# Performance work log

Hardware: AMD Instinct MI355X
Metric: run time of the kernel (lower is better)

## Reference

```python
import jax, jax.numpy as jnp
import numpy as np

B, S, D, H, E, K, F, FS = 4, 2048, 1024, 16, 8, 2, 4096, 2048
HD = D // H
EPS = 1e-5
T = B * S
CAP = int(1.25 * K * T / E)  # capacity factor 1.25 -> 2560 tokens/expert


def _ln(x, g, b):
    mu = jnp.mean(x, -1, keepdims=True)
    var = jnp.var(x, -1, keepdims=True)
    return (x - mu) * jax.lax.rsqrt(var + EPS) * g + b


def _forward(x, attention_mask, ln1_g, ln1_b, wq, bq, wk, bk, wv, bv, wo, bo,
             ln2_g, ln2_b, w_router, w1, b1, w2, b2, ws1, bs1, ws2, bs2):
    # ---- pre-LN self-attention + residual ----
    xn = _ln(x, ln1_g, ln1_b)
    q = (xn @ wq + bq).reshape(B, S, H, HD)
    k = (xn @ wk + bk).reshape(B, S, H, HD)
    v = (xn @ wv + bv).reshape(B, S, H, HD)
    scores = jnp.einsum('bqhd,bkhd->bhqk', q, k) / np.float32(np.sqrt(HD))
    scores = jnp.where(attention_mask[:, None, None, :], jnp.finfo(scores.dtype).min, scores)
    p = jax.nn.softmax(scores, axis=-1)
    attn = jnp.einsum('bhqk,bkhd->bqhd', p, v).reshape(B, S, D) @ wo + bo
    x = x + attn
    # ---- pre-LN sparse MoE FFN + residual ----
    xn = _ln(x, ln2_g, ln2_b).reshape(T, D)
    logits = xn.astype(jnp.float32) @ w_router              # router in fp32, [T,E]
    probs = jax.nn.softmax(logits, axis=-1)
    topv, topi = jax.lax.top_k(probs, K)                    # [T,K]
    topv = topv / jnp.sum(topv, -1, keepdims=True)          # renormalize top-k gates
    oh = jax.nn.one_hot(topi, E, dtype=jnp.float32)         # [T,K,E]
    flat = oh.transpose(1, 0, 2).reshape(K * T, E)          # slot-major routing priority
    pos_tok = jnp.sum((jnp.cumsum(flat, axis=0) - 1.0) * flat, -1)  # slot position within expert
    keep = pos_tok < CAP                                    # drop tokens over capacity
    posc = jnp.clip(pos_tok, 0, CAP - 1).astype(jnp.int32)
    eidx = topi.T.reshape(K * T)
    w = topv.T.reshape(K * T) * keep
    xt = jnp.tile(xn, (K, 1)) * keep[:, None]               # [K*T, D]
    disp = jnp.zeros((E, CAP, D), xn.dtype).at[eidx, posc].add(xt)   # dispatch [E,C,D]
    h = jax.nn.gelu(jnp.einsum('ecd,edf->ecf', disp, w1) + b1[:, None, :], approximate=False)
    eo = jnp.einsum('ecf,efd->ecd', h, w2) + b2[:, None, :]          # expert out [E,C,D]
    y = jnp.sum(eo[eidx, posc].reshape(K, T, D) * w.reshape(K, T, 1), axis=0)  # combine
    # shared expert (dense, always active)
    y = y + jax.nn.gelu(xn @ ws1 + bs1, approximate=False) @ ws2 + bs2
    return x + y.reshape(B, S, D)


def setup_inputs() -> dict:
    key = jax.random.key(0)
    ks = jax.random.split(key, 16)
    g = lambda k, shape, fan: jax.random.normal(k, shape, jnp.float32) * (fan ** -0.5)
    return {
        'x': jax.random.normal(ks[0], (B, S, D), jnp.float32),
        'attention_mask': jnp.zeros((B, S), bool),
        'ln1_g': jnp.ones((D,), jnp.float32), 'ln1_b': jnp.zeros((D,), jnp.float32),
        'wq': g(ks[1], (D, D), D), 'bq': jnp.zeros((D,), jnp.float32),
        'wk': g(ks[2], (D, D), D), 'bk': jnp.zeros((D,), jnp.float32),
        'wv': g(ks[3], (D, D), D), 'bv': jnp.zeros((D,), jnp.float32),
        'wo': g(ks[4], (D, D), D), 'bo': jnp.zeros((D,), jnp.float32),
        'ln2_g': jnp.ones((D,), jnp.float32), 'ln2_b': jnp.zeros((D,), jnp.float32),
        'w_router': g(ks[5], (D, E), D),
        'w1': g(ks[6], (E, D, F), D), 'b1': jnp.zeros((E, F), jnp.float32),
        'w2': g(ks[7], (E, F, D), F), 'b2': jnp.zeros((E, D), jnp.float32),
        'ws1': g(ks[8], (D, FS), D), 'bs1': jnp.zeros((FS,), jnp.float32),
        'ws2': g(ks[9], (FS, D), FS), 'bs2': jnp.zeros((D,), jnp.float32),
    }


def reference(x, attention_mask, ln1_g, ln1_b, wq, bq, wk, bk, wv, bv, wo, bo,
              ln2_g, ln2_b, w_router, w1, b1, w2, b2, ws1, bs1, ws2, bs2):
    return _forward(x, attention_mask, ln1_g, ln1_b, wq, bq, wk, bk, wv, bv, wo, bo,
                    ln2_g, ln2_b, w_router, w1, b1, w2, b2, ws1, bs1, ws2, bs2)
```

## Files before the change

kernel.cpp:

```cpp
#include <hip/hip_runtime.h>
#include <hip/hip_bf16.h>
#include <stdint.h>

#define D_ 1024
#define S_ 2048
#define B_ 4
#define H_ 16
#define T_ 8192
#define E_ 8
#define CAP_ 2560
#define F_ 4096
#define FS_ 2048

typedef __attribute__((ext_vector_type(8))) short s8v;
typedef __attribute__((ext_vector_type(4))) float f4v;

#define GLL(gp, lp) __builtin_amdgcn_global_load_lds( \
    (const __attribute__((address_space(1))) unsigned int*)(gp), \
    (__attribute__((address_space(3))) unsigned int*)(lp), 16, 0, 0)

__device__ inline short f2bf(float f) {
    union { float f; unsigned u; } v; v.f = f;
    unsigned r = (v.u + 0x7fffu + ((v.u >> 16) & 1u)) >> 16;
    return (short)(r & 0xffffu);
}
__device__ inline float b2f(short h) {
    union { unsigned u; float f; } v; v.u = ((unsigned)(unsigned short)h) << 16; return v.f;
}
__device__ inline float gelu_f(float x) {
    return 0.5f * x * (1.0f + erff(x * 0.7071067811865475f));
}
__device__ inline f4v f4zero() { f4v z; z[0]=0.f; z[1]=0.f; z[2]=0.f; z[3]=0.f; return z; }

__device__ inline unsigned pk2(float a, float b, unsigned* lo) {
    const short ha = f2bf(a), hb = f2bf(b);
    const short la = f2bf(a - b2f(ha)), lb = f2bf(b - b2f(hb));
    *lo = ((unsigned)(unsigned short)lb << 16) | (unsigned)(unsigned short)la;
    return ((unsigned)(unsigned short)hb << 16) | (unsigned)(unsigned short)ha;
}

__global__ __launch_bounds__(256) void transcvt(const float* __restrict__ in,
                                                short* __restrict__ out, int R, int C)
{
    __shared__ float tile[32][33];
    const int tid = threadIdx.x;
    const int tx = tid & 31, ty = tid >> 5;
    const long long ib = (long long)blockIdx.z * R * C;
    const int r0 = blockIdx.y * 32, c0 = blockIdx.x * 32;
#pragma unroll
    for (int i = 0; i < 4; i++)
        tile[ty + i * 8][tx] = in[ib + (long long)(r0 + ty + i * 8) * C + c0 + tx];
    __syncthreads();
#pragma unroll
    for (int i = 0; i < 4; i++)
        out[ib + (long long)(c0 + ty + i * 8) * R + r0 + tx] = f2bf(tile[tx][ty + i * 8]);
}

__global__ __launch_bounds__(256) void transcvt2(const float* __restrict__ in,
    short* __restrict__ oh, short* __restrict__ ol, int R, int C)
{
    __shared__ float tile[32][33];
    const int tid = threadIdx.x;
    const int tx = tid & 31, ty = tid >> 5;
    const int r0 = blockIdx.y * 32, c0 = blockIdx.x * 32;
#pragma unroll
    for (int i = 0; i < 4; i++)
        tile[ty + i * 8][tx] = in[(long long)(r0 + ty + i * 8) * C + c0 + tx];
    __syncthreads();
#pragma unroll
    for (int i = 0; i < 4; i++) {
        const float v = tile[tx][ty + i * 8];
        const short h = f2bf(v);
        const long long o = (long long)(c0 + ty + i * 8) * R + r0 + tx;
        oh[o] = h;
        ol[o] = f2bf(v - b2f(h));
    }
}

__global__ __launch_bounds__(256) void ln1_split(const float* __restrict__ x,
    const float* __restrict__ g, const float* __restrict__ bta,
    short* __restrict__ xh, short* __restrict__ xl)
{
    const int t = blockIdx.x, tid = threadIdx.x;
    const float4 v = ((const float4*)(x + (long long)t * D_))[tid];
    float s1 = v.x + v.y + v.z + v.w;
    float s2 = v.x * v.x + v.y * v.y + v.z * v.z + v.w * v.w;
#pragma unroll
    for (int off = 32; off; off >>= 1) { s1 += __shfl_xor(s1, off, 64); s2 += __shfl_xor(s2, off, 64); }
    __shared__ float r1[4], r2[4];
    if ((tid & 63) == 0) { r1[tid >> 6] = s1; r2[tid >> 6] = s2; }
    __syncthreads();
    s1 = r1[0] + r1[1] + r1[2] + r1[3];
    s2 = r2[0] + r2[1] + r2[2] + r2[3];
    const float mu = s1 * (1.0f / D_);
    const float var = s2 * (1.0f / D_) - mu * mu;
    const float rs = rsqrtf(var + 1e-5f);
    const float4 gv = ((const float4*)g)[tid];
    const float4 bv = ((const float4*)bta)[tid];
    float xn[4];
    xn[0] = (v.x - mu) * rs * gv.x + bv.x;
    xn[1] = (v.y - mu) * rs * gv.y + bv.y;
    xn[2] = (v.z - mu) * rs * gv.z + bv.z;
    xn[3] = (v.w - mu) * rs * gv.w + bv.w;
    short4 hh, ll;
    hh.x = f2bf(xn[0]); ll.x = f2bf(xn[0] - b2f(hh.x));
    hh.y = f2bf(xn[1]); ll.y = f2bf(xn[1] - b2f(hh.y));
    hh.z = f2bf(xn[2]); ll.z = f2bf(xn[2] - b2f(hh.z));
    hh.w = f2bf(xn[3]); ll.w = f2bf(xn[3] - b2f(hh.w));
    ((short4*)(xh + (long long)t * D_))[tid] = hh;
    ((short4*)(xl + (long long)t * D_))[tid] = ll;
}

__global__ __launch_bounds__(256) void ln2_router_kernel(const float* __restrict__ x,
    const float* __restrict__ g, const float* __restrict__ bta, const float* __restrict__ wr,
    short* __restrict__ xo, int* __restrict__ topi, float* __restrict__ gates)
{
    const int t = blockIdx.x, tid = threadIdx.x;
    const float4 v = ((const float4*)(x + (long long)t * D_))[tid];
    float s1 = v.x + v.y + v.z + v.w;
    float s2 = v.x * v.x + v.y * v.y + v.z * v.z + v.w * v.w;
#pragma unroll
    for (int off = 32; off; off >>= 1) { s1 += __shfl_xor(s1, off, 64); s2 += __shfl_xor(s2, off, 64); }
    __shared__ float r1[4], r2[4];
    if ((tid & 63) == 0) { r1[tid >> 6] = s1; r2[tid >> 6] = s2; }
    __syncthreads();
    s1 = r1[0] + r1[1] + r1[2] + r1[3];
    s2 = r2[0] + r2[1] + r2[2] + r2[3];
    const float mu = s1 * (1.0f / D_);
    const float var = s2 * (1.0f / D_) - mu * mu;
    const float rs = rsqrtf(var + 1e-5f);
    const float4 gv = ((const float4*)g)[tid];
    const float4 bv = ((const float4*)bta)[tid];
    float xn[4];
    xn[0] = (v.x - mu) * rs * gv.x + bv.x;
    xn[1] = (v.y - mu) * rs * gv.y + bv.y;
    xn[2] = (v.z - mu) * rs * gv.z + bv.z;
    xn[3] = (v.w - mu) * rs * gv.w + bv.w;
    short4 o;
    o.x = f2bf(xn[0]); o.y = f2bf(xn[1]); o.z = f2bf(xn[2]); o.w = f2bf(xn[3]);
    ((short4*)(xo + (long long)t * D_))[tid] = o;

    float a8[8] = {0, 0, 0, 0, 0, 0, 0, 0};
#pragma unroll
    for (int q = 0; q < 4; q++) {
        const int d = tid * 4 + q;
        const float4 w0 = ((const float4*)(wr + d * 8))[0];
        const float4 w1 = ((const float4*)(wr + d * 8))[1];
        a8[0] += xn[q] * w0.x; a8[1] += xn[q] * w0.y; a8[2] += xn[q] * w0.z; a8[3] += xn[q] * w0.w;
        a8[4] += xn[q] * w1.x; a8[5] += xn[q] * w1.y; a8[6] += xn[q] * w1.z; a8[7] += xn[q] * w1.w;
    }
    __shared__ float lred[32];
#pragma unroll
    for (int e = 0; e < 8; e++) {
        float vv = a8[e];
#pragma unroll
        for (int off = 32; off; off >>= 1) vv += __shfl_xor(vv, off, 64);
        if ((tid & 63) == 0) lred[(tid >> 6) * 8 + e] = vv;
    }
    __syncthreads();
    if (tid == 0) {
        float lg[8];
#pragma unroll
        for (int e = 0; e < 8; e++) lg[e] = lred[e] + lred[8 + e] + lred[16 + e] + lred[24 + e];
        int e0 = 0;
        for (int e = 1; e < 8; e++) if (lg[e] > lg[e0]) e0 = e;
        int e1 = (e0 == 0) ? 1 : 0;
        for (int e = 0; e < 8; e++) if (e != e0 && lg[e] > lg[e1]) e1 = e;
        const float mx = lg[e0];
        float den = 0.f;
        for (int e = 0; e < 8; e++) den += expf(lg[e] - mx);
        const float p0 = expf(lg[e0] - mx) / den;
        const float p1 = expf(lg[e1] - mx) / den;
        const float inv = 1.0f / (p0 + p1);
        topi[t * 2] = e0; topi[t * 2 + 1] = e1;
        gates[t * 2] = p0 * inv; gates[t * 2 + 1] = p1 * inv;
    }
}

__global__ __launch_bounds__(256) void route_scan(const int* __restrict__ topi,
    const float* __restrict__ gates, int* __restrict__ posc, float* __restrict__ wv)
{
    const int tid = threadIdx.x;
    const int w = tid >> 6, lane = tid & 63;
    __shared__ int wsum[4 * 8];
    int cnt[8] = {0, 0, 0, 0, 0, 0, 0, 0};
    const int base_r = tid * 64;
    for (int i = 0; i < 64; i++) {
        const int r = base_r + i;
        const int k = r >> 13, t = r & (T_ - 1);
        cnt[topi[t * 2 + k]]++;
    }
    int excl[8];
#pragma unroll
    for (int e = 0; e < 8; e++) {
        int x = cnt[e];
#pragma unroll
        for (int off = 1; off < 64; off <<= 1) {
            int y = __shfl_up(x, off, 64);
            if (lane >= off) x += y;
        }
        excl[e] = x - cnt[e];
        if (lane == 63) wsum[w * 8 + e] = x;
    }
    __syncthreads();
    int pos[8];
#pragma unroll
    for (int e = 0; e < 8; e++) {
        int s = 0;
        for (int ww = 0; ww < 4; ww++) if (ww < w) s += wsum[ww * 8 + e];
        pos[e] = s + excl[e];
    }
    for (int i = 0; i < 64; i++) {
        const int r = base_r + i;
        const int k = r >> 13, t = r & (T_ - 1);
        const int e = topi[t * 2 + k];
        const int p = pos[e]++;
        const bool keep = p < CAP_;
        posc[r] = keep ? p : -1;
        wv[r] = keep ? gates[t * 2 + k] : 0.0f;
    }
}

__global__ __launch_bounds__(128) void dispatch_kernel(const short* __restrict__ xn2,
    const int* __restrict__ topi, const int* __restrict__ posc, short* __restrict__ disp)
{
    const int r = blockIdx.x;
    const int p = posc[r];
    if (p < 0) return;
    const int k = r >> 13, t = r & (T_ - 1);
    const int e = topi[t * 2 + k];
    const int tid = threadIdx.x;
    *(s8v*)&disp[((long long)e * CAP_ + p) * D_ + tid * 8] =
        *(const s8v*)&xn2[(long long)t * D_ + tid * 8];
}

__global__ __launch_bounds__(256) void combine_kernel(const float* __restrict__ x1,
    const float* __restrict__ ys, const float* __restrict__ eo,
    const int* __restrict__ topi, const int* __restrict__ posc,
    const float* __restrict__ wv, float* __restrict__ out)
{
    const int t = blockIdx.x, tid = threadIdx.x;
    float4 a = *(const float4*)&x1[(long long)t * D_ + tid * 4];
    const float4 b = *(const float4*)&ys[(long long)t * D_ + tid * 4];
    a.x += b.x; a.y += b.y; a.z += b.z; a.w += b.w;
#pragma unroll
    for (int k = 0; k < 2; k++) {
        const int r = k * T_ + t;
        const int p = posc[r];
        if (p >= 0) {
            const int e = topi[t * 2 + k];
            const float wt = wv[r];
            const float4 c = *(const float4*)&eo[((long long)e * CAP_ + p) * D_ + tid * 4];
            a.x += wt * c.x; a.y += wt * c.y; a.z += wt * c.z; a.w += wt * c.w;
        }
    }
    *(float4*)&out[(long long)t * D_ + tid * 4] = a;
}

template <int EPI>
__global__ __launch_bounds__(256) void gemm_btz(
    const short* __restrict__ A, const short* __restrict__ Bt,
    const float* __restrict__ bias, void* __restrict__ Cout,
    int M, int N, int K, int ldc,
    long long sA, long long sB, long long sBias, long long sC)
{
    __shared__ __align__(16) short lA[128 * 32];
    __shared__ __align__(16) short lB[128 * 32];
    const int z = blockIdx.z;
    A += (long long)z * sA;
    Bt += (long long)z * sB;
    bias += (long long)z * sBias;
    const int tid = threadIdx.x;
    const int wvi = tid >> 6, lane = tid & 63, lid = lane & 15, quad = lane >> 4;
    const int wm = wvi >> 1, wn = wvi & 1;
    const int mBase = blockIdx.y * 128, nBase = blockIdx.x * 128;
    f4v acc[4][4];
#pragma unroll
    for (int i = 0; i < 4; i++)
#pragma unroll
        for (int j = 0; j < 4; j++) acc[i][j] = f4zero();
    const long long aOff0 = (long long)(mBase + (tid >> 2)) * K + (tid & 3) * 8;
    const long long aOff1 = aOff0 + 64LL * K;
    const long long bOff0 = (long long)(nBase + (tid >> 2)) * K + (tid & 3) * 8;
    const long long bOff1 = bOff0 + 64LL * K;
    const int wofs = wvi << 9;
    for (int k0 = 0; k0 < K; k0 += 32) {
        __syncthreads();
        GLL(A + aOff0 + k0, &lA[wofs]);  GLL(A + aOff1 + k0, &lA[2048 + wofs]);
        GLL(Bt + bOff0 + k0, &lB[wofs]); GLL(Bt + bOff1 + k0, &lB[2048 + wofs]);
        __syncthreads();
        s8v af[4], bf[4];
#pragma unroll
        for (int i = 0; i < 4; i++)
            af[i] = *(const s8v*)&lA[(wm * 64 + i * 16 + lid) * 32 + quad * 8];
#pragma unroll
        for (int j = 0; j < 4; j++)
            bf[j] = *(const s8v*)&lB[(wn * 64 + j * 16 + lid) * 32 + quad * 8];
#pragma unroll
        for (int i = 0; i < 4; i++)
#pragma unroll
            for (int j = 0; j < 4; j++)
                acc[i][j] = __builtin_amdgcn_mfma_f32_16x16x32_bf16(af[i], bf[j], acc[i][j], 0, 0, 0);
    }
    const int mW = mBase + wm * 64 + quad * 4;
    const int nW = nBase + wn * 64 + lid;
    short* Cs = (short*)Cout + (long long)z * sC;
    float* Cf = (float*)Cout + (long long)z * sC;
#pragma unroll
    for (int j = 0; j < 4; j++) {
        const int n = nW + j * 16;
        const float bn = bias[n];
#pragma unroll
        for (int i = 0; i < 4; i++) {
            const int m = mW + i * 16;
#pragma unroll
            for (int r = 0; r < 4; r++) {
                float v = acc[i][j][r] + bn;
                if (EPI == 1) { v = gelu_f(v); Cs[(long long)(m + r) * ldc + n] = f2bf(v); }
                else          { Cf[(long long)(m + r) * ldc + n] = v; }
            }
        }
    }
}

template <int EPI>
__global__ __launch_bounds__(256) void gemm_hl(
    const short* __restrict__ Ah, const short* __restrict__ Al,
    const short* __restrict__ Bh, const short* __restrict__ Bl,
    const float* __restrict__ biasQ, const float* __restrict__ biasK,
    const float* __restrict__ biasV, const float* __restrict__ resid,
    short* __restrict__ Ch, short* __restrict__ Cl, float* __restrict__ Cf,
    int M, int N, int K, int ldc)
{
    __shared__ __align__(16) short lAh[4096], lAl[4096], lBh[4096], lBl[4096];
    const int tid = threadIdx.x;
    const int wvi = tid >> 6, lane = tid & 63, lid = lane & 15, quad = lane >> 4;
    const int wm = wvi >> 1, wn = wvi & 1;
    const int mBase = blockIdx.y * 128, nBase = blockIdx.x * 128;
    f4v acc[4][4];
#pragma unroll
    for (int i = 0; i < 4; i++)
#pragma unroll
        for (int j = 0; j < 4; j++) acc[i][j] = f4zero();
    const long long aOff0 = (long long)(mBase + (tid >> 2)) * K + (tid & 3) * 8;
    const long long aOff1 = aOff0 + 64LL * K;
    const long long bOff0 = (long long)(nBase + (tid >> 2)) * K + (tid & 3) * 8;
    const long long bOff1 = bOff0 + 64LL * K;
    const int wofs = wvi << 9;
    for (int k0 = 0; k0 < K; k0 += 32) {
        __syncthreads();
        GLL(Ah + aOff0 + k0, &lAh[wofs]);  GLL(Ah + aOff1 + k0, &lAh[2048 + wofs]);
        GLL(Al + aOff0 + k0, &lAl[wofs]);  GLL(Al + aOff1 + k0, &lAl[2048 + wofs]);
        GLL(Bh + bOff0 + k0, &lBh[wofs]);  GLL(Bh + bOff1 + k0, &lBh[2048 + wofs]);
        GLL(Bl + bOff0 + k0, &lBl[wofs]);  GLL(Bl + bOff1 + k0, &lBl[2048 + wofs]);
        __syncthreads();
        s8v ah[4], al[4], bh[4], bl[4];
#pragma unroll
        for (int i = 0; i < 4; i++) {
            const int ro = (wm * 64 + i * 16 + lid) * 32 + quad * 8;
            ah[i] = *(const s8v*)&lAh[ro];
            al[i] = *(const s8v*)&lAl[ro];
        }
#pragma unroll
        for (int j = 0; j < 4; j++) {
            const int ro = (wn * 64 + j * 16 + lid) * 32 + quad * 8;
            bh[j] = *(const s8v*)&lBh[ro];
            bl[j] = *(const s8v*)&lBl[ro];
        }
#pragma unroll
        for (int i = 0; i < 4; i++)
#pragma unroll
            for (int j = 0; j < 4; j++) {
                acc[i][j] = __builtin_amdgcn_mfma_f32_16x16x32_bf16(ah[i], bh[j], acc[i][j], 0, 0, 0);
                acc[i][j] = __builtin_amdgcn_mfma_f32_16x16x32_bf16(ah[i], bl[j], acc[i][j], 0, 0, 0);
                acc[i][j] = __builtin_amdgcn_mfma_f32_16x16x32_bf16(al[i], bh[j], acc[i][j], 0, 0, 0);
            }
    }
    const int mW = mBase + wm * 64 + quad * 4;
    const int nW = nBase + wn * 64 + lid;
#pragma unroll
    for (int j = 0; j < 4; j++) {
        const int n = nW + j * 16;
        const float* bp = (n < 1024) ? biasQ : ((n < 2048) ? biasK : biasV);
        const float bn = bp[n & 1023];
#pragma unroll
        for (int i = 0; i < 4; i++) {
            const int m = mW + i * 16;
#pragma unroll
            for (int r = 0; r < 4; r++) {
                const float v = acc[i][j][r] + bn;
                const long long o = (long long)(m + r) * ldc + n;
                if (EPI == 0) {
                    const short h = f2bf(v);
                    Ch[o] = h;
                    Cl[o] = f2bf(v - b2f(h));
                } else {
                    Cf[o] = v + resid[o];
                }
            }
        }
    }
}

__global__ __launch_bounds__(256) void flash_attn_hl(const short* __restrict__ qkvh,
    const short* __restrict__ qkvl, const unsigned char* __restrict__ mask,
    short* __restrict__ attnh, short* __restrict__ attnl)
{
    __shared__ __align__(16) short lKh[32 * 72], lKl[32 * 72];
    __shared__ __align__(16) short lVth[64 * 40], lVtl[64 * 40];
    const int tid = threadIdx.x;
    const int lane = tid & 63, lid = lane & 15, quad = lane >> 4;
    const int w = tid >> 6;
    const int bh = blockIdx.y;
    const int b = bh >> 4, h = bh & 15;
    const int q0row = blockIdx.x * 64 + w * 16;

    const long long rowQ = (long long)(b * S_ + q0row + lid) * 3072 + h * 64;
    const s8v qh0 = *(const s8v*)&qkvh[rowQ + quad * 8];
    const s8v qh1 = *(const s8v*)&qkvh[rowQ + 32 + quad * 8];
    const s8v ql0 = *(const s8v*)&qkvl[rowQ + quad * 8];
    const s8v ql1 = *(const s8v*)&qkvl[rowQ + 32 + quad * 8];

    float m_run = -1e30f, l_run = 0.0f;
    f4v o[4];
#pragma unroll
    for (int dt = 0; dt < 4; dt++) o[dt] = f4zero();

    const unsigned char* mrow = mask + b * S_;
    const int srow = tid >> 3, sgrp = tid & 7;
    const int vcol = srow ^ ((sgrp & 3) << 3);
    const int srcA = lid + ((quad & 1) << 5);
    const int srcB = srcA + 16;

    s8v kh_r, kl_r, vh_r, vl_r;
    {
        const long long gk = (long long)(b * S_ + srow) * 3072 + 1024 + h * 64 + sgrp * 8;
        kh_r = *(const s8v*)&qkvh[gk];
        kl_r = *(const s8v*)&qkvl[gk];
        vh_r = *(const s8v*)&qkvh[gk + 1024];
        vl_r = *(const s8v*)&qkvl[gk + 1024];
    }

    for (int c0 = 0; c0 < S_; c0 += 32) {
        __syncthreads();
        {
            *(s8v*)&lKh[srow * 72 + sgrp * 8] = kh_r;
            *(s8v*)&lKl[srow * 72 + sgrp * 8] = kl_r;
#pragma unroll
            for (int jj = 0; jj < 8; jj++) {
                lVth[(sgrp * 8 + jj) * 40 + vcol] = vh_r[jj];
                lVtl[(sgrp * 8 + jj) * 40 + vcol] = vl_r[jj];
            }
        }
        __syncthreads();
        if (c0 + 32 < S_) {
            const long long gk = (long long)(b * S_ + c0 + 32 + srow) * 3072 + 1024 + h * 64 + sgrp * 8;
            kh_r = *(const s8v*)&qkvh[gk];
            kl_r = *(const s8v*)&qkvl[gk];
            vh_r = *(const s8v*)&qkvh[gk + 1024];
            vl_r = *(const s8v*)&qkvl[gk + 1024];
        }

        f4v s0 = f4zero(), s1 = f4zero();
        {
            const int r0 = lid * 72 + quad * 8;
            const s8v kh0a = *(const s8v*)&lKh[r0];
            const s8v kh0b = *(const s8v*)&lKh[r0 + 32];
            const s8v kl0a = *(const s8v*)&lKl[r0];
            const s8v kl0b = *(const s8v*)&lKl[r0 + 32];
            const int r1i = (16 + lid) * 72 + quad * 8;
            const s8v kh1a = *(const s8v*)&lKh[r1i];
            const s8v kh1b = *(const s8v*)&lKh[r1i + 32];
            const s8v kl1a = *(const s8v*)&lKl[r1i];
            const s8v kl1b = *(const s8v*)&lKl[r1i + 32];
            __builtin_amdgcn_s_setprio(1);
            s0 = __builtin_amdgcn_mfma_f32_16x16x32_bf16(kh0a, qh0, s0, 0, 0, 0);
            s0 = __builtin_amdgcn_mfma_f32_16x16x32_bf16(kh0b, qh1, s0, 0, 0, 0);
            s0 = __builtin_amdgcn_mfma_f32_16x16x32_bf16(kl0a, qh0, s0, 0, 0, 0);
            s0 = __builtin_amdgcn_mfma_f32_16x16x32_bf16(kl0b, qh1, s0, 0, 0, 0);
            s0 = __builtin_amdgcn_mfma_f32_16x16x32_bf16(kh0a, ql0, s0, 0, 0, 0);
            s0 = __builtin_amdgcn_mfma_f32_16x16x32_bf16(kh0b, ql1, s0, 0, 0, 0);
            s1 = __builtin_amdgcn_mfma_f32_16x16x32_bf16(kh1a, qh0, s1, 0, 0, 0);
            s1 = __builtin_amdgcn_mfma_f32_16x16x32_bf16(kh1b, qh1, s1, 0, 0, 0);
            s1 = __builtin_amdgcn_mfma_f32_16x16x32_bf16(kl1a, qh0, s1, 0, 0, 0);
            s1 = __builtin_amdgcn_mfma_f32_16x16x32_bf16(kl1b, qh1, s1, 0, 0, 0);
            s1 = __builtin_amdgcn_mfma_f32_16x16x32_bf16(kh1a, ql0, s1, 0, 0, 0);
            s1 = __builtin_amdgcn_mfma_f32_16x16x32_bf16(kh1b, ql1, s1, 0, 0, 0);
            __builtin_amdgcn_s_setprio(0);
        }
        const unsigned mm0 = *(const unsigned*)(mrow + c0 + quad * 4);
        const unsigned mm1 = *(const unsigned*)(mrow + c0 + 16 + quad * 4);
        float p[8];
#pragma unroll
        for (int r = 0; r < 4; r++) {
            p[r]     = ((mm0 >> (8 * r)) & 255u) ? -1e30f : s0[r] * 0.125f;
            p[4 + r] = ((mm1 >> (8 * r)) & 255u) ? -1e30f : s1[r] * 0.125f;
        }
        float mx = fmaxf(fmaxf(fmaxf(p[0], p[1]), fmaxf(p[2], p[3])),
                         fmaxf(fmaxf(p[4], p[5]), fmaxf(p[6], p[7])));
        mx = fmaxf(mx, __shfl_xor(mx, 16, 64));
        mx = fmaxf(mx, __shfl_xor(mx, 32, 64));
        if (__all(mx - m_run <= 8.0f)) {
            float rs = 0.0f;
#pragma unroll
            for (int i = 0; i < 8; i++) { p[i] = __expf(p[i] - m_run); rs += p[i]; }
            rs += __shfl_xor(rs, 16, 64);
            rs += __shfl_xor(rs, 32, 64);
            l_run += rs;
        } else {
            const float mn = fmaxf(m_run, mx);
            const float alpha = __expf(m_run - mn);
            m_run = mn;
            float rs = 0.0f;
#pragma unroll
            for (int i = 0; i < 8; i++) { p[i] = __expf(p[i] - mn); rs += p[i]; }
            rs += __shfl_xor(rs, 16, 64);
            rs += __shfl_xor(rs, 32, 64);
            l_run = l_run * alpha + rs;
#pragma unroll
            for (int dt = 0; dt < 4; dt++)
#pragma unroll
                for (int r = 0; r < 4; r++) o[dt][r] *= alpha;
        }

        unsigned c0l, c1l, c2l, c3l;
        const unsigned c0h = pk2(p[0], p[1], &c0l);
        const unsigned c1h = pk2(p[2], p[3], &c1l);
        const unsigned c2h = pk2(p[4], p[5], &c2l);
        const unsigned c3h = pk2(p[6], p[7], &c3l);
        union { s8v v; unsigned u[4]; } pah, pal;
        {
            const unsigned a0 = __shfl((int)c0h, srcA, 64), a2 = __shfl((int)c2h, srcA, 64);
            const unsigned a1 = __shfl((int)c1h, srcA, 64), a3 = __shfl((int)c3h, srcA, 64);
            const unsigned b0 = __shfl((int)c0h, srcB, 64), b2 = __shfl((int)c2h, srcB, 64);
            const unsigned b1 = __shfl((int)c1h, srcB, 64), b3 = __shfl((int)c3h, srcB, 64);
            const bool lo = (quad < 2);
            pah.u[0] = lo ? a0 : a2; pah.u[1] = lo ? a1 : a3;
            pah.u[2] = lo ? b0 : b2; pah.u[3] = lo ? b1 : b3;
        }
        {
            const unsigned a0 = __shfl((int)c0l, srcA, 64), a2 = __shfl((int)c2l, srcA, 64);
            const unsigned a1 = __shfl((int)c1l, srcA, 64), a3 = __shfl((int)c3l, srcA, 64);
            const unsigned b0 = __shfl((int)c0l, srcB, 64), b2 = __shfl((int)c2l, srcB, 64);
            const unsigned b1 = __shfl((int)c1l, srcB, 64), b3 = __shfl((int)c3l, srcB, 64);
            const bool lo = (quad < 2);
            pal.u[0] = lo ? a0 : a2; pal.u[1] = lo ? a1 : a3;
            pal.u[2] = lo ? b0 : b2; pal.u[3] = lo ? b1 : b3;
        }

        __builtin_amdgcn_s_setprio(1);
#pragma unroll
        for (int dt = 0; dt < 4; dt++) {
            const int d = dt * 16 + lid;
            const int x3 = (dt * 2 + (lid >> 3)) & 3;
            const int ro = d * 40 + ((quad ^ x3) << 3);
            const s8v bvh = *(const s8v*)&lVth[ro];
            const s8v bvl = *(const s8v*)&lVtl[ro];
            o[dt] = __builtin_amdgcn_mfma_f32_16x16x32_bf16(bvh, pah.v, o[dt], 0, 0, 0);
            o[dt] = __builtin_amdgcn_mfma_f32_16x16x32_bf16(bvl, pah.v, o[dt], 0, 0, 0);
            o[dt] = __builtin_amdgcn_mfma_f32_16x16x32_bf16(bvh, pal.v, o[dt], 0, 0, 0);
        }
        __builtin_amdgcn_s_setprio(0);
    }
    const float inv_l = 1.0f / l_run;
    const long long obase = (long long)(b * S_ + q0row + lid) * D_ + h * 64 + quad * 4;
#pragma unroll
    for (int dt = 0; dt < 4; dt++) {
        short4 hh4, ll4;
        float v0 = o[dt][0] * inv_l, v1 = o[dt][1] * inv_l;
        float v2 = o[dt][2] * inv_l, v3 = o[dt][3] * inv_l;
        hh4.x = f2bf(v0); ll4.x = f2bf(v0 - b2f(hh4.x));
        hh4.y = f2bf(v1); ll4.y = f2bf(v1 - b2f(hh4.y));
        hh4.z = f2bf(v2); ll4.z = f2bf(v2 - b2f(hh4.z));
        hh4.w = f2bf(v3); ll4.w = f2bf(v3 - b2f(hh4.w));
        *(short4*)&attnh[obase + dt * 16] = hh4;
        *(short4*)&attnl[obase + dt * 16] = ll4;
    }
}

constexpr long long SZ_DD2   = (long long)D_ * D_ * 2;
constexpr long long OFF_WQKVH = 0;
constexpr long long OFF_WQKVL = OFF_WQKVH + 3 * SZ_DD2;
constexpr long long OFF_WOH   = OFF_WQKVL + 3 * SZ_DD2;
constexpr long long OFF_WOL   = OFF_WOH + SZ_DD2;
constexpr long long OFF_W1T   = OFF_WOL + SZ_DD2;
constexpr long long OFF_W2T   = OFF_W1T + (long long)E_ * F_ * D_ * 2;
constexpr long long OFF_WS1T  = OFF_W2T + (long long)E_ * D_ * F_ * 2;
constexpr long long OFF_WS2T  = OFF_WS1T + (long long)FS_ * D_ * 2;
constexpr long long OFF_X1    = OFF_WS2T + (long long)D_ * FS_ * 2;
constexpr long long OFF_XN2   = OFF_X1 + (long long)T_ * D_ * 4;
constexpr long long OFF_TOPI  = OFF_XN2 + (long long)T_ * D_ * 2;
constexpr long long OFF_GATES = OFF_TOPI + (long long)T_ * 2 * 4;
constexpr long long OFF_POSC  = OFF_GATES + (long long)T_ * 2 * 4;
constexpr long long OFF_WVAL  = OFF_POSC + (long long)2 * T_ * 4;
constexpr long long ZONE      = OFF_WVAL + (long long)2 * T_ * 4;
constexpr long long OFF_XH1   = ZONE;
constexpr long long OFF_XL1   = OFF_XH1 + (long long)T_ * D_ * 2;
constexpr long long OFF_QKVH  = OFF_XL1 + (long long)T_ * D_ * 2;
constexpr long long OFF_QKVL  = OFF_QKVH + (long long)T_ * 3 * D_ * 2;
constexpr long long OFF_ATTNH = OFF_QKVL + (long long)T_ * 3 * D_ * 2;
constexpr long long OFF_ATTNL = OFF_ATTNH + (long long)T_ * D_ * 2;
constexpr long long OFF_DISP  = ZONE;
constexpr long long OFF_H     = OFF_DISP + (long long)E_ * CAP_ * D_ * 2;
constexpr long long OFF_EO    = OFF_H + (long long)4 * CAP_ * F_ * 2;
constexpr long long OFF_YS    = OFF_EO + (long long)E_ * CAP_ * D_ * 4;
constexpr long long OFF_HS    = ZONE;

extern "C" void kernel_launch(void* const* d_in, const int* in_sizes, int n_in,
                              void* d_out, int out_size, void* d_ws, size_t ws_size,
                              hipStream_t stream)
{
    (void)in_sizes; (void)n_in; (void)out_size; (void)ws_size;
    const float* x       = (const float*)d_in[0];
    const unsigned char* mask = (const unsigned char*)d_in[1];
    const float* ln1g    = (const float*)d_in[2];
    const float* ln1b    = (const float*)d_in[3];
    const float* wq      = (const float*)d_in[4];
    const float* bq      = (const float*)d_in[5];
    const float* wk      = (const float*)d_in[6];
    const float* bk      = (const float*)d_in[7];
    const float* wvp     = (const float*)d_in[8];
    const float* bvv     = (const float*)d_in[9];
    const float* wo      = (const float*)d_in[10];
    const float* bo      = (const float*)d_in[11];
    const float* ln2g    = (const float*)d_in[12];
    const float* ln2b    = (const float*)d_in[13];
    const float* wrouter = (const float*)d_in[14];
    const float* w1      = (const float*)d_in[15];
    const float* b1      = (const float*)d_in[16];
    const float* w2      = (const float*)d_in[17];
    const float* b2      = (const float*)d_in[18];
    const float* ws1     = (const float*)d_in[19];
    const float* bs1     = (const float*)d_in[20];
    const float* ws2     = (const float*)d_in[21];
    const float* bs2     = (const float*)d_in[22];
    float* out = (float*)d_out;
    char* ws = (char*)d_ws;

    short* wqkvh = (short*)(ws + OFF_WQKVH);
    short* wqkvl = (short*)(ws + OFF_WQKVL);
    short* woh   = (short*)(ws + OFF_WOH);
    short* wol   = (short*)(ws + OFF_WOL);
    short* w1T   = (short*)(ws + OFF_W1T);
    short* w2T   = (short*)(ws + OFF_W2T);
    short* ws1T  = (short*)(ws + OFF_WS1T);
    short* ws2T  = (short*)(ws + OFF_WS2T);
    float* x1    = (float*)(ws + OFF_X1);
    short* xn2   = (short*)(ws + OFF_XN2);
    int*   topi  = (int*)(ws + OFF_TOPI);
    float* gates = (float*)(ws + OFF_GATES);
    int*   posc  = (int*)(ws + OFF_POSC);
    float* wval  = (float*)(ws + OFF_WVAL);
    short* xh1   = (short*)(ws + OFF_XH1);
    short* xl1   = (short*)(ws + OFF_XL1);
    short* qkvh  = (short*)(ws + OFF_QKVH);
    short* qkvl  = (short*)(ws + OFF_QKVL);
    short* attnh = (short*)(ws + OFF_ATTNH);
    short* attnl = (short*)(ws + OFF_ATTNL);
    short* disp  = (short*)(ws + OFF_DISP);
    short* hbuf  = (short*)(ws + OFF_H);
    float* eo    = (float*)(ws + OFF_EO);
    short* hs    = (short*)(ws + OFF_HS);
    float* ysb   = (float*)(ws + OFF_YS);

    const dim3 tb(256);
    transcvt2<<<dim3(32, 32), tb, 0, stream>>>(wq,  wqkvh,               wqkvl,               1024, 1024);
    transcvt2<<<dim3(32, 32), tb, 0, stream>>>(wk,  wqkvh + 1024 * 1024, wqkvl + 1024 * 1024, 1024, 1024);
    transcvt2<<<dim3(32, 32), tb, 0, stream>>>(wvp, wqkvh + 2 * 1024 * 1024, wqkvl + 2 * 1024 * 1024, 1024, 1024);
    transcvt2<<<dim3(32, 32), tb, 0, stream>>>(wo,  woh, wol, 1024, 1024);
    transcvt<<<dim3(128, 32, 8), tb, 0, stream>>>(w1, w1T, 1024, 4096);
    transcvt<<<dim3(32, 128, 8), tb, 0, stream>>>(w2, w2T, 4096, 1024);
    transcvt<<<dim3(64, 32, 1), tb, 0, stream>>>(ws1, ws1T, 1024, 2048);
    transcvt<<<dim3(32, 64, 1), tb, 0, stream>>>(ws2, ws2T, 2048, 1024);

    ln1_split<<<T_, 256, 0, stream>>>(x, ln1g, ln1b, xh1, xl1);

    gemm_hl<0><<<dim3(24, 64), 256, 0, stream>>>(xh1, xl1, wqkvh, wqkvl,
        bq, bk, bvv, nullptr, qkvh, qkvl, nullptr, T_, 3072, 1024, 3072);

    flash_attn_hl<<<dim3(32, 64), 256, 0, stream>>>(qkvh, qkvl, mask, attnh, attnl);

    gemm_hl<1><<<dim3(8, 64), 256, 0, stream>>>(attnh, attnl, woh, wol,
        bo, bo, bo, x, nullptr, nullptr, x1, T_, 1024, 1024, 1024);

    ln2_router_kernel<<<T_, 256, 0, stream>>>(x1, ln2g, ln2b, wrouter, xn2, topi, gates);
    route_scan<<<1, 256, 0, stream>>>(topi, gates, posc, wval);
    dispatch_kernel<<<2 * T_, 128, 0, stream>>>(xn2, topi, posc, disp);

    for (int g = 0; g < 2; g++) {
        const long long e0 = (long long)g * 4;
        gemm_btz<1><<<dim3(32, 20, 4), 256, 0, stream>>>(
            disp + e0 * CAP_ * D_, w1T + e0 * F_ * D_, b1 + e0 * F_, hbuf,
            CAP_, F_, 1024, F_,
            (long long)CAP_ * D_, (long long)F_ * D_, (long long)F_, (long long)CAP_ * F_);
        gemm_btz<2><<<dim3(8, 20, 4), 256, 0, stream>>>(
            hbuf, w2T + e0 * D_ * F_, b2 + e0 * D_, eo + e0 * CAP_ * D_,
            CAP_, 1024, F_, 1024,
            (long long)CAP_ * F_, (long long)D_ * F_, (long long)D_, (long long)CAP_ * D_);
    }

    gemm_btz<1><<<dim3(16, 64, 1), 256, 0, stream>>>(xn2, ws1T, bs1, hs,
        T_, FS_, 1024, FS_, 0, 0, 0, 0);
    gemm_btz<2><<<dim3(8, 64, 1), 256, 0, stream>>>(hs, ws2T, bs2, ysb,
        T_, 1024, FS_, 1024, 0, 0, 0, 0);

    combine_kernel<<<T_, 256, 0, stream>>>(x1, ysb, eo, topi, posc, wval, out);
}
```

Before: 1.891 ms.

## Add XCD block swizzle to GEMMs, exp2 softmax and hardware bf16 packing in attention

Remaps GEMM workgroup indices so that consecutive tiles land on the same XCD, aiming to improve L2 reuse on the multi-die GPU. In flash attention, the scale and rescale threshold are folded into log2 space so exp2f can replace __expf. The software bf16 hi/lo split is replaced with the v_cvt_pk_bf16_f32 instruction to cut ALU work in the softmax and output paths. The swizzle only applies when the grid size is a multiple of 8. The packing instruction's rounding must match the software round-to-nearest-even for results to stay identical.

```diff
diff --git a/kernel.cpp b/kernel.cpp
--- a/kernel.cpp
+++ b/kernel.cpp
@@ -32,11 +32,29 @@
 }
 __device__ inline f4v f4zero() { f4v z; z[0]=0.f; z[1]=0.f; z[2]=0.f; z[3]=0.f; return z; }
 
-__device__ inline unsigned pk2(float a, float b, unsigned* lo) {
-    const short ha = f2bf(a), hb = f2bf(b);
-    const short la = f2bf(a - b2f(ha)), lb = f2bf(b - b2f(hb));
-    *lo = ((unsigned)(unsigned short)lb << 16) | (unsigned)(unsigned short)la;
-    return ((unsigned)(unsigned short)hb << 16) | (unsigned)(unsigned short)ha;
+__device__ inline unsigned cvtpk(float a, float b) {
+    unsigned r;
+    asm("v_cvt_pk_bf16_f32 %0, %1, %2" : "=v"(r) : "v"(a), "v"(b));
+    return r;
+}
+__device__ inline float ubits2f(unsigned u) {
+    union { unsigned u; float f; } v; v.u = u; return v.f;
+}
+__device__ inline void pk2c(float a, float b, unsigned* hi, unsigned* lo) {
+    const unsigned h = cvtpk(a, b);
+    const float fa = ubits2f(h << 16);
+    const float fb = ubits2f(h & 0xffff0000u);
+    *lo = cvtpk(a - fa, b - fb);
+    *hi = h;
+}
+
+__device__ inline void xcd_swizzle(int gx, int gy, int& bx, int& by) {
+    const int nwg = gx * gy;
+    if (nwg & 7) return;
+    int bid = by * gx + bx;
+    bid = (bid & 7) * (nwg >> 3) + (bid >> 3);
+    by = bid / gx;
+    bx = bid - by * gx;
 }
 
 __global__ __launch_bounds__(256) void transcvt(const float* __restrict__ in,
@@ -273,7 +291,9 @@
     const int tid = threadIdx.x;
     const int wvi = tid >> 6, lane = tid & 63, lid = lane & 15, quad = lane >> 4;
     const int wm = wvi >> 1, wn = wvi & 1;
-    const int mBase = blockIdx.y * 128, nBase = blockIdx.x * 128;
+    int bx = blockIdx.x, by = blockIdx.y;
+    xcd_swizzle(gridDim.x, gridDim.y, bx, by);
+    const int mBase = by * 128, nBase = bx * 128;
     f4v acc[4][4];
 #pragma unroll
     for (int i = 0; i < 4; i++)
@@ -336,7 +356,9 @@
     const int tid = threadIdx.x;
     const int wvi = tid >> 6, lane = tid & 63, lid = lane & 15, quad = lane >> 4;
     const int wm = wvi >> 1, wn = wvi & 1;
-    const int mBase = blockIdx.y * 128, nBase = blockIdx.x * 128;
+    int bx = blockIdx.x, by = blockIdx.y;
+    xcd_swizzle(gridDim.x, gridDim.y, bx, by);
+    const int mBase = by * 128, nBase = bx * 128;
     f4v acc[4][4];
 #pragma unroll
     for (int i = 0; i < 4; i++)
@@ -415,13 +437,16 @@
     const int b = bh >> 4, h = bh & 15;
     const int q0row = blockIdx.x * 64 + w * 16;
 
+    const float SC2 = 0.125f * 1.44269504088896f;
+    const float THR2 = 8.0f * 1.44269504088896f;
+
     const long long rowQ = (long long)(b * S_ + q0row + lid) * 3072 + h * 64;
     const s8v qh0 = *(const s8v*)&qkvh[rowQ + quad * 8];
     const s8v qh1 = *(const s8v*)&qkvh[rowQ + 32 + quad * 8];
     const s8v ql0 = *(const s8v*)&qkvl[rowQ + quad * 8];
     const s8v ql1 = *(const s8v*)&qkvl[rowQ + 32 + quad * 8];
 
-    float m_run = -1e30f, l_run = 0.0f;
+    float m2_run = -1e30f, l_run = 0.0f;
     f4v o[4];
 #pragma unroll
     for (int dt = 0; dt < 4; dt++) o[dt] = f4zero();
@@ -493,27 +518,27 @@
         float p[8];
 #pragma unroll
         for (int r = 0; r < 4; r++) {
-            p[r]     = ((mm0 >> (8 * r)) & 255u) ? -1e30f : s0[r] * 0.125f;
-            p[4 + r] = ((mm1 >> (8 * r)) & 255u) ? -1e30f : s1[r] * 0.125f;
-        }
-        float mx = fmaxf(fmaxf(fmaxf(p[0], p[1]), fmaxf(p[2], p[3])),
-                         fmaxf(fmaxf(p[4], p[5]), fmaxf(p[6], p[7])));
+            p[r]     = ((mm0 >> (8 * r)) & 255u) ? -1e30f : s0[r] * SC2;
+            p[4 + r] = ((mm1 >> (8 * r)) & 255u) ? -1e30f : s1[r] * SC2;
+        }
+        float mx = fmaxf(fmaxf(fmaxf(p[0], p[1]), p[2]), fmaxf(fmaxf(p[3], p[4]), p[5]));
+        mx = fmaxf(fmaxf(mx, p[6]), p[7]);
         mx = fmaxf(mx, __shfl_xor(mx, 16, 64));
         mx = fmaxf(mx, __shfl_xor(mx, 32, 64));
-        if (__all(mx - m_run <= 8.0f)) {
+        if (__all(mx - m2_run <= THR2)) {
             float rs = 0.0f;
 #pragma unroll
-            for (int i = 0; i < 8; i++) { p[i] = __expf(p[i] - m_run); rs += p[i]; }
+            for (int i = 0; i < 8; i++) { p[i] = exp2f(p[i] - m2_run); rs += p[i]; }
             rs += __shfl_xor(rs, 16, 64);
             rs += __shfl_xor(rs, 32, 64);
             l_run += rs;
         } else {
-            const float mn = fmaxf(m_run, mx);
-            const float alpha = __expf(m_run - mn);
-            m_run = mn;
+            const float mn = fmaxf(m2_run, mx);
+            const float alpha = exp2f(m2_run - mn);
+            m2_run = mn;
             float rs = 0.0f;
 #pragma unroll
-            for (int i = 0; i < 8; i++) { p[i] = __expf(p[i] - mn); rs += p[i]; }
+            for (int i = 0; i < 8; i++) { p[i] = exp2f(p[i] - mn); rs += p[i]; }
             rs += __shfl_xor(rs, 16, 64);
             rs += __shfl_xor(rs, 32, 64);
             l_run = l_run * alpha + rs;
@@ -523,11 +548,11 @@
                 for (int r = 0; r < 4; r++) o[dt][r] *= alpha;
         }
 
-        unsigned c0l, c1l, c2l, c3l;
-        const unsigned c0h = pk2(p[0], p[1], &c0l);
-        const unsigned c1h = pk2(p[2], p[3], &c1l);
-        const unsigned c2h = pk2(p[4], p[5], &c2l);
-        const unsigned c3h = pk2(p[6], p[7], &c3l);
+        unsigned c0h, c1h, c2h, c3h, c0l, c1l, c2l, c3l;
+        pk2c(p[0], p[1], &c0h, &c0l);
+        pk2c(p[2], p[3], &c1h, &c1l);
+        pk2c(p[4], p[5], &c2h, &c2l);
+        pk2c(p[6], p[7], &c3h, &c3l);
         union { s8v v; unsigned u[4]; } pah, pal;
         {
             const unsigned a0 = __shfl((int)c0h, srcA, 64), a2 = __shfl((int)c2h, srcA, 64);
@@ -566,15 +591,16 @@
     const long long obase = (long long)(b * S_ + q0row + lid) * D_ + h * 64 + quad * 4;
 #pragma unroll
     for (int dt = 0; dt < 4; dt++) {
-        short4 hh4, ll4;
-        float v0 = o[dt][0] * inv_l, v1 = o[dt][1] * inv_l;
-        float v2 = o[dt][2] * inv_l, v3 = o[dt][3] * inv_l;
-        hh4.x = f2bf(v0); ll4.x = f2bf(v0 - b2f(hh4.x));
-        hh4.y = f2bf(v1); ll4.y = f2bf(v1 - b2f(hh4.y));
-        hh4.z = f2bf(v2); ll4.z = f2bf(v2 - b2f(hh4.z));
-        hh4.w = f2bf(v3); ll4.w = f2bf(v3 - b2f(hh4.w));
-        *(short4*)&attnh[obase + dt * 16] = hh4;
-        *(short4*)&attnl[obase + dt * 16] = ll4;
+        const float v0 = o[dt][0] * inv_l, v1 = o[dt][1] * inv_l;
+        const float v2 = o[dt][2] * inv_l, v3 = o[dt][3] * inv_l;
+        unsigned h01, l01, h23, l23;
+        pk2c(v0, v1, &h01, &l01);
+        pk2c(v2, v3, &h23, &l23);
+        uint2 hh, ll;
+        hh.x = h01; hh.y = h23;
+        ll.x = l01; ll.y = l23;
+        *(uint2*)&attnh[obase + dt * 16] = hh;
+        *(uint2*)&attnl[obase + dt * 16] = ll;
     }
 }
 
```

Result: no change. 1.908 ms (+0.9%).
